# Kernel optimization log

Measured on AMD Instinct MI355X. Metric: run time of the kernel, lower is better.

## Reference

```python
import jax, jax.numpy as jnp
import numpy as np
from jax import lax

B, CIN, H, W = 32, 256, 56, 56
COUT, M, K = 256, 2, 3
CMID = COUT * M  # 512
SPARSITY = 0.9


def _make_binary_weight(key):
    k1, k2 = jax.random.split(key)
    shape = (CMID, CIN, K, K)
    mask = jax.random.bernoulli(k1, SPARSITY, shape)
    sign = jax.random.bernoulli(k2, 0.5, shape).astype(jnp.float32) * 2.0 - 1.0
    return jnp.where(mask, sign, 0.0).astype(jnp.float32)


def setup_inputs() -> dict:
    key = jax.random.key(0)
    kx, kw, kfw, kfb = jax.random.split(key, 4)
    x = jax.random.normal(kx, (B, CIN, H, W), dtype=jnp.float32)
    binary_w = _make_binary_weight(kw)
    fan_in = CMID  # 1x1 conv fan-in
    bound = 1.0 / np.sqrt(fan_in)
    fc_w = jax.random.uniform(kfw, (COUT, CMID, 1, 1), minval=-bound, maxval=bound, dtype=jnp.float32)
    fc_b = jax.random.uniform(kfb, (COUT,), minval=-bound, maxval=bound, dtype=jnp.float32)
    return {"x": x, "binary_w": binary_w, "fc_w": fc_w, "fc_b": fc_b}


def reference(x, binary_w, fc_w, fc_b):
    pad = K // 2
    # fixed random ternary conv, stride 1, same padding
    y = lax.conv_general_dilated(
        x, binary_w, window_strides=(1, 1), padding=[(pad, pad), (pad, pad)],
        dimension_numbers=("NCHW", "OIHW", "NCHW"))
    y = jax.nn.relu(y)
    # learnable 1x1 conv with bias
    y = lax.conv_general_dilated(
        y, fc_w, window_strides=(1, 1), padding=[(0, 0), (0, 0)],
        dimension_numbers=("NCHW", "OIHW", "NCHW"))
    return y + fc_b[None, :, None, None]
```

## Files before the change

### kernel.cpp

```cpp
#include <hip/hip_runtime.h>
#include <hip/hip_bf16.h>
#include <stdint.h>


typedef __attribute__((ext_vector_type(8))) short short8;
typedef __attribute__((ext_vector_type(4))) float floatx4;

#define ROWE 8192
#define PLANE (58*ROWE)
#define NT_PER_B 28

#define OFF_WP  0
#define OFF_A2  2359296
#define OFF_XP  2621440
#define OFF_Y   63439872

__device__ static inline void async16(const void* gptr, void* lptr) {
  __builtin_amdgcn_global_load_lds(
      (const __attribute__((address_space(1))) void*)gptr,
      (__attribute__((address_space(3))) void*)lptr,
      16, 0, 0);
}

__device__ static inline unsigned short f2bf(float x) {
  __hip_bfloat16 h = __float2bfloat16(x);
  return *reinterpret_cast<unsigned short*>(&h);
}

__global__ void k_xprep(const float* __restrict__ x, __hip_bfloat16* __restrict__ Xp) {
  const int idx = blockIdx.x * 256 + threadIdx.x;
  const int klo = idx & 7;
  const int wq  = (idx >> 3) & 63;
  const int khi = (idx >> 9) & 15;
  const int t2  = idx >> 13;
  const int hp  = t2 % 58;
  const int bc  = t2 / 58;
  const int b   = bc >> 1;
  const int cin = ((bc & 1) << 7) + (khi << 3) + klo;
  const int h = hp - 1, w = wq - 1;
  float v = 0.f;
  if ((unsigned)h < 56u && (unsigned)w < 56u)
    v = x[((b * 256 + cin) * 56 + h) * 56 + w];
  Xp[idx] = __float2bfloat16(v);
}

__global__ void k_wprep(const float* __restrict__ bw, __hip_bfloat16* __restrict__ Wp) {
  const int idx = blockIdx.x * 256 + threadIdx.x;
  const int klo = idx & 7;
  const int cml = (idx >> 3) & 63;
  const int khi = (idx >> 9) & 15;
  const int cmh = (idx >> 13) & 1;
  const int rest = idx >> 14;
  const int cmblk = rest & 3;
  const int tcg = rest >> 2;
  const int cg  = tcg & 1;
  const int tap = tcg >> 1;
  const int kh = tap / 3, kw = tap - kh * 3;
  const int cm  = (cmblk << 7) + (cmh << 6) + cml;
  const int cin = (cg << 7) + (khi << 3) + klo;
  Wp[idx] = __float2bfloat16(bw[((cm * 256 + cin) * 3 + kh) * 3 + kw]);
}

__global__ void k_a2prep(const float* __restrict__ fw, __hip_bfloat16* __restrict__ A2) {
  const int idx = blockIdx.x * 256 + threadIdx.x;
  const int klo = idx & 7;
  const int cl  = (idx >> 3) & 63;
  const int khi = (idx >> 9) & 15;
  const int ch  = (idx >> 13) & 1;
  const int rest = idx >> 14;
  const int mtile = rest & 1;
  const int cg = rest >> 1;
  const int cout = (mtile << 7) + (ch << 6) + cl;
  const int cm   = (cg << 7) + (khi << 3) + klo;
  A2[idx] = __float2bfloat16(fw[cout * 512 + cm]);
}

__global__ __launch_bounds__(256, 2) void k_conv1(
    const __hip_bfloat16* __restrict__ Xp, const __hip_bfloat16* __restrict__ Wp,
    __hip_bfloat16* __restrict__ Y) {
  __shared__ short8 lds_raw[4096];
  char* lds = (char*)lds_raw;
  const int tid  = threadIdx.x;
  const int lane = tid & 63;
  const int wv   = tid >> 6;
  const int wm   = wv >> 1, wn = wv & 1;
  const int l15  = lane & 15;
  const int quad = lane >> 4;
  const int cmblk = blockIdx.x;
  const int ntile = blockIdx.y;
  const int b  = ntile / NT_PER_B;
  const int h0 = (ntile % NT_PER_B) * 2;

  floatx4 acc[4][4];
#pragma unroll
  for (int i = 0; i < 4; i++)
#pragma unroll
    for (int j = 0; j < 4; j++) acc[i][j] = (floatx4){0.f, 0.f, 0.f, 0.f};

  for (int t = 0; t < 18; ++t) {
    const int tap = t >> 1;
    const int cg  = t & 1;
    const int kh = tap / 3, kw = tap - kh * 3;
    const size_t a_base = (size_t)((tap * 2 + cg) * 4 + cmblk) * 16384;
    const size_t b_base = (size_t)((b * 2 + cg) * 58 + (h0 + kh)) * ROWE + kw * 8;
    __syncthreads();
    const char* gA = (const char*)(Wp + a_base) + wv * 8192 + lane * 16;
    const char* gB = (const char*)(Xp + b_base) + wv * 8192 + lane * 16;
    char* lA = lds + wv * 8192;
    char* lB = lds + 32768 + wv * 8192;
#pragma unroll
    for (int c = 0; c < 8; ++c) {
      async16(gA + c * 1024, lA + c * 1024);
      async16(gB + c * 1024, lB + c * 1024);
    }
    __syncthreads();
#pragma unroll
    for (int kk = 0; kk < 4; ++kk) {
      short8 af[4], bf[4];
#pragma unroll
      for (int mi = 0; mi < 4; ++mi) {
        const int m = wm * 64 + mi * 16 + l15;
        af[mi] = *(const short8*)(lds + ((m >> 6) * 16 + kk * 4 + quad) * 1024 + (m & 63) * 16);
      }
#pragma unroll
      for (int ni = 0; ni < 4; ++ni) {
        const int n = wn * 64 + ni * 16 + l15;
        bf[ni] = *(const short8*)(lds + 32768 + ((n >> 6) * 16 + kk * 4 + quad) * 1024 + (n & 63) * 16);
      }
#pragma unroll
      for (int mi = 0; mi < 4; ++mi)
#pragma unroll
        for (int ni = 0; ni < 4; ++ni)
          acc[mi][ni] = __builtin_amdgcn_mfma_f32_16x16x32_bf16(af[mi], bf[ni], acc[mi][ni], 0, 0, 0);
    }
  }

  const size_t ybase = ((size_t)ntile * 4 + cmblk) * 16384;
#pragma unroll
  for (int mi = 0; mi < 4; ++mi) {
    const int cml  = wm * 64 + mi * 16 + quad * 4;
    const int khi  = cml >> 3;
    const int klo0 = cml & 7;
#pragma unroll
    for (int ni = 0; ni < 4; ++ni) {
      const int n = wn * 64 + ni * 16 + l15;
      const int r = n >> 6, w = n & 63;
      floatx4 f = acc[mi][ni];
      unsigned lo = (unsigned)f2bf(fmaxf(f[0], 0.f)) | ((unsigned)f2bf(fmaxf(f[1], 0.f)) << 16);
      unsigned hi = (unsigned)f2bf(fmaxf(f[2], 0.f)) | ((unsigned)f2bf(fmaxf(f[3], 0.f)) << 16);
      uint2 pk = make_uint2(lo, hi);
      *(uint2*)((char*)Y + (ybase + (size_t)r * 8192 + khi * 512 + w * 8 + klo0) * 2) = pk;
    }
  }
}

__global__ __launch_bounds__(256, 2) void k_conv2(
    const __hip_bfloat16* __restrict__ Y, const __hip_bfloat16* __restrict__ A2,
    const float* __restrict__ fcb, float* __restrict__ out) {
  __shared__ short8 lds_raw[4096];
  char* lds = (char*)lds_raw;
  const int tid  = threadIdx.x;
  const int lane = tid & 63;
  const int wv   = tid >> 6;
  const int wm   = wv >> 1, wn = wv & 1;
  const int l15  = lane & 15;
  const int quad = lane >> 4;
  const int mtile = blockIdx.x;
  const int rp    = blockIdx.y;

  floatx4 acc[4][4];
#pragma unroll
  for (int i = 0; i < 4; i++)
#pragma unroll
    for (int j = 0; j < 4; j++) acc[i][j] = (floatx4){0.f, 0.f, 0.f, 0.f};

  for (int cg = 0; cg < 4; ++cg) {
    const size_t a_base = (size_t)(cg * 2 + mtile) * 16384;
    const size_t b_base = (size_t)(rp * 4 + cg) * 16384;
    __syncthreads();
    const char* gA = (const char*)(A2 + a_base) + wv * 8192 + lane * 16;
    const char* gB = (const char*)(Y + b_base) + wv * 8192 + lane * 16;
    char* lA = lds + wv * 8192;
    char* lB = lds + 32768 + wv * 8192;
#pragma unroll
    for (int c = 0; c < 8; ++c) {
      async16(gA + c * 1024, lA + c * 1024);
      async16(gB + c * 1024, lB + c * 1024);
    }
    __syncthreads();
#pragma unroll
    for (int kk = 0; kk < 4; ++kk) {
      short8 af[4], bf[4];
#pragma unroll
      for (int mi = 0; mi < 4; ++mi) {
        const int m = wm * 64 + mi * 16 + l15;
        af[mi] = *(const short8*)(lds + ((m >> 6) * 16 + kk * 4 + quad) * 1024 + (m & 63) * 16);
      }
#pragma unroll
      for (int ni = 0; ni < 4; ++ni) {
        const int n = wn * 64 + ni * 16 + l15;
        bf[ni] = *(const short8*)(lds + 32768 + ((n >> 6) * 16 + kk * 4 + quad) * 1024 + (n & 63) * 16);
      }
#pragma unroll
      for (int mi = 0; mi < 4; ++mi)
#pragma unroll
        for (int ni = 0; ni < 4; ++ni)
          acc[mi][ni] = __builtin_amdgcn_mfma_f32_16x16x32_bf16(af[mi], bf[ni], acc[mi][ni], 0, 0, 0);
    }
  }

  const int b   = rp / NT_PER_B;
  const int nb0 = (rp % NT_PER_B) * 128;
#pragma unroll
  for (int mi = 0; mi < 4; ++mi) {
    const int co = mtile * 128 + wm * 64 + mi * 16 + quad * 4;
#pragma unroll
    for (int ni = 0; ni < 4; ++ni) {
      const int n = wn * 64 + ni * 16 + l15;
      const int w = n & 63;
      if (w < 56) {
        const int nb = nb0 + n;
        const int h  = nb >> 6;
        floatx4 f = acc[mi][ni];
        const size_t base = (size_t)(b * 256 + co) * 3136 + h * 56 + w;
#pragma unroll
        for (int r = 0; r < 4; ++r)
          out[base + (size_t)r * 3136] = f[r] + fcb[co + r];
      }
    }
  }
}

extern "C" void kernel_launch(void* const* d_in, const int* in_sizes, int n_in,
                              void* d_out, int out_size, void* d_ws, size_t ws_size,
                              hipStream_t stream) {
  const float* x  = (const float*)d_in[0];
  const float* bw = (const float*)d_in[1];
  const float* fw = (const float*)d_in[2];
  const float* fb = (const float*)d_in[3];
  float* out = (float*)d_out;
  char* ws = (char*)d_ws;

  __hip_bfloat16* Wp = (__hip_bfloat16*)(ws + OFF_WP);
  __hip_bfloat16* A2 = (__hip_bfloat16*)(ws + OFF_A2);
  __hip_bfloat16* Xp = (__hip_bfloat16*)(ws + OFF_XP);
  __hip_bfloat16* Y  = (__hip_bfloat16*)(ws + OFF_Y);

  k_wprep<<<dim3(4608), dim3(256), 0, stream>>>(bw, Wp);
  k_a2prep<<<dim3(512), dim3(256), 0, stream>>>(fw, A2);
  k_xprep<<<dim3(118784), dim3(256), 0, stream>>>(x, Xp);
  k_conv1<<<dim3(4, 896), dim3(256), 0, stream>>>(Xp, Wp, Y);
  k_conv2<<<dim3(2, 896), dim3(256), 0, stream>>>(Y, A2, fb, out);
}
```

Before: 528.0 us.

## Vectorize input prep and remap conv blocks for XCD-local L2 reuse

The input-prep kernel now has each thread gather 8 channels and write one 16-byte packed store, replacing one scalar bf16 store per thread and cutting the thread count by 8x. Both GEMM kernels switch to a 1D grid whose block index is remapped so that consecutive blocks on the same XCD share spatial tiles and all channel blocks of a tile land on one XCD. This aims to improve L2 hit rates on the chiplet GPU. The per-thread input reads are strided by a channel plane, which may reduce coalescing compared with the old contiguous reads.

```diff
diff --git a/kernel.cpp b/kernel.cpp
--- a/kernel.cpp
+++ b/kernel.cpp
@@ -7,7 +7,6 @@
 typedef __attribute__((ext_vector_type(4))) float floatx4;
 
 #define ROWE 8192
-#define PLANE (58*ROWE)
 #define NT_PER_B 28
 
 #define OFF_WP  0
@@ -28,20 +27,30 @@
 }
 
 __global__ void k_xprep(const float* __restrict__ x, __hip_bfloat16* __restrict__ Xp) {
-  const int idx = blockIdx.x * 256 + threadIdx.x;
-  const int klo = idx & 7;
-  const int wq  = (idx >> 3) & 63;
-  const int khi = (idx >> 9) & 15;
-  const int t2  = idx >> 13;
+  const int t = blockIdx.x * 256 + threadIdx.x;
+  const int wq  = t & 63;
+  const int khi = (t >> 6) & 15;
+  const int t2  = t >> 10;
   const int hp  = t2 % 58;
   const int bc  = t2 / 58;
   const int b   = bc >> 1;
-  const int cin = ((bc & 1) << 7) + (khi << 3) + klo;
+  const int cin0 = ((bc & 1) << 7) + (khi << 3);
   const int h = hp - 1, w = wq - 1;
-  float v = 0.f;
-  if ((unsigned)h < 56u && (unsigned)w < 56u)
-    v = x[((b * 256 + cin) * 56 + h) * 56 + w];
-  Xp[idx] = __float2bfloat16(v);
+  unsigned short v[8];
+  if ((unsigned)h < 56u && (unsigned)w < 56u) {
+    const float* xp = x + ((size_t)(b * 256 + cin0) * 56 + h) * 56 + w;
+#pragma unroll
+    for (int j = 0; j < 8; ++j) v[j] = f2bf(xp[(size_t)j * 3136]);
+  } else {
+#pragma unroll
+    for (int j = 0; j < 8; ++j) v[j] = 0;
+  }
+  uint4 pk;
+  pk.x = (unsigned)v[0] | ((unsigned)v[1] << 16);
+  pk.y = (unsigned)v[2] | ((unsigned)v[3] << 16);
+  pk.z = (unsigned)v[4] | ((unsigned)v[5] << 16);
+  pk.w = (unsigned)v[6] | ((unsigned)v[7] << 16);
+  *(uint4*)(Xp + (size_t)t * 8) = pk;
 }
 
 __global__ void k_wprep(const float* __restrict__ bw, __hip_bfloat16* __restrict__ Wp) {
@@ -86,8 +95,11 @@
   const int wm   = wv >> 1, wn = wv & 1;
   const int l15  = lane & 15;
   const int quad = lane >> 4;
-  const int cmblk = blockIdx.x;
-  const int ntile = blockIdx.y;
+  const int id   = blockIdx.x;
+  const int xcd  = id & 7;
+  const int seq  = id >> 3;
+  const int cmblk = seq & 3;
+  const int ntile = xcd * 112 + (seq >> 2);
   const int b  = ntile / NT_PER_B;
   const int h0 = (ntile % NT_PER_B) * 2;
 
@@ -165,8 +177,11 @@
   const int wm   = wv >> 1, wn = wv & 1;
   const int l15  = lane & 15;
   const int quad = lane >> 4;
-  const int mtile = blockIdx.x;
-  const int rp    = blockIdx.y;
+  const int id   = blockIdx.x;
+  const int xcd  = id & 7;
+  const int seq  = id >> 3;
+  const int mtile = seq & 1;
+  const int rp    = xcd * 112 + (seq >> 1);
 
   floatx4 acc[4][4];
 #pragma unroll
@@ -248,7 +263,7 @@
 
   k_wprep<<<dim3(4608), dim3(256), 0, stream>>>(bw, Wp);
   k_a2prep<<<dim3(512), dim3(256), 0, stream>>>(fw, A2);
-  k_xprep<<<dim3(118784), dim3(256), 0, stream>>>(x, Xp);
-  k_conv1<<<dim3(4, 896), dim3(256), 0, stream>>>(Xp, Wp, Y);
-  k_conv2<<<dim3(2, 896), dim3(256), 0, stream>>>(Y, A2, fb, out);
-}
+  k_xprep<<<dim3(14848), dim3(256), 0, stream>>>(x, Xp);
+  k_conv1<<<dim3(3584), dim3(256), 0, stream>>>(Xp, Wp, Y);
+  k_conv2<<<dim3(1792), dim3(256), 0, stream>>>(Y, A2, fb, out);
+}
```

After: 474.3 us. 10.2% less time.
